# Optimization experiments

Measured on AMD Instinct MI355X. Metric: run time of the kernel, lower is better.

The kernel has to match this reference:

```python
import jax, jax.numpy as jnp
import numpy as np

B, T, D, H = 8, 1024, 1024, 16

def setup_inputs() -> dict:
    key = jax.random.key(0)
    k1, k2, k3, k4, k5 = jax.random.split(key, 5)
    x = jax.random.normal(k1, (B, T, D), dtype=jnp.float32)
    mask = jnp.tril(jnp.ones((T, T), dtype=bool))[None, None]  # [1,1,T,T] causal
    s = 0.02
    W_attn = jax.random.normal(k2, (D, 3 * D), dtype=jnp.float32) * s
    b_attn = jnp.zeros((3 * D,), dtype=jnp.float32)
    W_proj = jax.random.normal(k3, (D, D), dtype=jnp.float32) * s
    b_proj = jnp.zeros((D,), dtype=jnp.float32)
    return {"x": x, "mask": mask, "W_attn": W_attn, "b_attn": b_attn,
            "W_proj": W_proj, "b_proj": b_proj}

def reference(x, mask, W_attn, b_attn, W_proj, b_proj):
    num_heads = H
    b, t, d = x.shape
    hd = d // num_heads
    qkv = x @ W_attn + b_attn                      # [b,t,3d]
    q, k, v = jnp.split(qkv, 3, axis=-1)
    def to_heads(a):
        return a.reshape(b, t, num_heads, hd).transpose(0, 2, 1, 3)  # [b,h,t,hd]
    q, k, v = to_heads(q), to_heads(k), to_heads(v)
    scale = 1.0 / jnp.sqrt(jnp.float32(hd))
    attn = jnp.einsum('bhqd,bhkd->bhqk', q, k) * scale
    attn = jnp.where(mask, attn, jnp.finfo(jnp.float32).min)
    attn = jax.nn.softmax(attn, axis=-1)
    o = jnp.einsum('bhqk,bhkd->bhqd', attn, v)
    o = o.transpose(0, 2, 1, 3).reshape(b, t, d)   # [b,t,d]
    return o @ W_proj + b_proj
```

## Files before the change

### kernel.cpp

```cpp
#include <hip/hip_runtime.h>
#include <cstdint>


typedef __attribute__((ext_vector_type(8))) short bf16x8;
typedef __attribute__((ext_vector_type(4))) float f32x4;

__device__ __forceinline__ short f2b(float x) {
  unsigned u = __builtin_bit_cast(unsigned, x);
  u += 0x7fffu + ((u >> 16) & 1u);
  return (short)(u >> 16);
}

__device__ __forceinline__ void gl2lds16(short* l, const short* g) {
  __builtin_amdgcn_global_load_lds(
      (const __attribute__((address_space(1))) void*)g,
      (__attribute__((address_space(3))) void*)l, 16, 0, 0);
}


__global__ void f32_to_bf16_vec(const float* __restrict__ in,
                                short* __restrict__ outb, int n4) {
  int i = blockIdx.x * 256 + threadIdx.x;
  if (i >= n4) return;
  float4 v = ((const float4*)in)[i];
  short4 o;
  o.x = f2b(v.x); o.y = f2b(v.y); o.z = f2b(v.z); o.w = f2b(v.w);
  ((short4*)outb)[i] = o;
}

__global__ void transpose_f32_bf16(const float* __restrict__ in,
                                   short* __restrict__ out, int R, int C) {
  __shared__ float tile[32][33];
  int c0 = blockIdx.x * 32, r0 = blockIdx.y * 32;
  int tx = threadIdx.x, ty = threadIdx.y;
#pragma unroll
  for (int i = 0; i < 32; i += 8)
    tile[ty + i][tx] = in[(long)(r0 + ty + i) * C + c0 + tx];
  __syncthreads();
#pragma unroll
  for (int i = 0; i < 32; i += 8)
    out[(long)(c0 + ty + i) * R + r0 + tx] = f2b(tile[tx][ty + i]);
}


__global__ __launch_bounds__(512, 2) void gemm_qkv256(
    const short* __restrict__ A, const short* __restrict__ Bt,
    const float* __restrict__ bias,
    short* __restrict__ qh, short* __restrict__ kh, short* __restrict__ vT,
    int M, int N, int K) {
  __shared__ short As[2][256 * 64];
  __shared__ short Bs[2][256 * 64];
  const int t = threadIdx.x;
  const int wave = t >> 6, lane = t & 63;
  const int quad = lane >> 4, l15 = lane & 15;
  const int wm = wave >> 2, wn = wave & 3;

  const int nx = gridDim.x;
  const int bid0 = blockIdx.y * nx + blockIdx.x;
  const int cpx = (nx * gridDim.y) >> 3;
  const int bid = (bid0 & 7) * cpx + (bid0 >> 3);
  const int n0 = (bid % nx) * 256;
  const int m0 = (bid / nx) * 256;

  f32x4 acc[8][4] = {};

  const int srow = t >> 3;
  const int sch = (t & 7) ^ (srow & 7);
  const short* aS = A + (long)(m0 + srow) * K + sch * 8;
  const short* bS = Bt + (long)(n0 + srow) * K + sch * 8;
  const long rK = (long)64 * K;

  const int sw0 = (quad ^ (l15 & 7)) * 8;
  const int sw1 = ((4 + quad) ^ (l15 & 7)) * 8;
  const short* aF = &As[0][(wm * 128 + l15) * 64];
  const short* bF = &Bs[0][(wn * 64 + l15) * 64];
  const int BUF = 256 * 64;

  const int ntiles = K >> 6;

  {
    short* ad = &As[0][t * 8];
    short* bd = &Bs[0][t * 8];
    gl2lds16(bd, bS);
    gl2lds16(bd + 4096, bS + rK);
    gl2lds16(bd + 2 * 4096, bS + 2 * rK);
    gl2lds16(bd + 3 * 4096, bS + 3 * rK);
    gl2lds16(ad, aS);
    gl2lds16(ad + 2 * 4096, aS + 2 * rK);
    gl2lds16(ad + 4096, aS + rK);
    gl2lds16(ad + 3 * 4096, aS + 3 * rK);
  }
  asm volatile("s_waitcnt vmcnt(2)" ::: "memory");
  __builtin_amdgcn_s_barrier();

#pragma unroll 1
  for (int kt = 0; kt < ntiles - 1; ++kt) {
    const int cur = kt & 1;
    const short* Ab = aF + cur * BUF;
    const short* Bb = bF + cur * BUF;
    short* ad = &As[cur ^ 1][t * 8];
    short* bd = &Bs[cur ^ 1][t * 8];
    const short* aN = aS + (long)(kt + 1) * 64;
    const short* bN = bS + (long)(kt + 1) * 64;
#pragma unroll
    for (int ph = 0; ph < 4; ++ph) {
      const int mh = ph >> 1;
      const int sw = (ph & 1) ? sw1 : sw0;
      bf16x8 af[4], bf[4];
#pragma unroll
      for (int i = 0; i < 4; ++i)
        af[i] = *(const bf16x8*)(Ab + (mh * 64 + i * 16) * 64 + sw);
#pragma unroll
      for (int j = 0; j < 4; ++j)
        bf[j] = *(const bf16x8*)(Bb + j * 16 * 64 + sw);
      if (ph == 0) { gl2lds16(bd, bN); gl2lds16(bd + 4096, bN + rK); }
      if (ph == 1) { gl2lds16(bd + 2 * 4096, bN + 2 * rK);
                     gl2lds16(bd + 3 * 4096, bN + 3 * rK); }
      if (ph == 2) { gl2lds16(ad, aN); gl2lds16(ad + 2 * 4096, aN + 2 * rK); }
      if (ph == 3) { gl2lds16(ad + 4096, aN + rK);
                     gl2lds16(ad + 3 * 4096, aN + 3 * rK); }
      __builtin_amdgcn_s_barrier();
      asm volatile("s_waitcnt lgkmcnt(0)" ::: "memory");
      __builtin_amdgcn_sched_barrier(0);
      __builtin_amdgcn_s_setprio(1);
#pragma unroll
      for (int i = 0; i < 4; ++i)
#pragma unroll
        for (int j = 0; j < 4; ++j)
          acc[mh * 4 + i][j] = __builtin_amdgcn_mfma_f32_16x16x32_bf16(
              af[i], bf[j], acc[mh * 4 + i][j], 0, 0, 0);
      __builtin_amdgcn_s_setprio(0);
      if (ph == 1) asm volatile("s_waitcnt vmcnt(4)" ::: "memory");
      if (ph == 3) asm volatile("s_waitcnt vmcnt(2)" ::: "memory");
      __builtin_amdgcn_s_barrier();
    }
  }

  {
    const int cur = (ntiles - 1) & 1;
    const short* Ab = aF + cur * BUF;
    const short* Bb = bF + cur * BUF;
#pragma unroll
    for (int ph = 0; ph < 4; ++ph) {
      const int mh = ph >> 1;
      const int sw = (ph & 1) ? sw1 : sw0;
      bf16x8 af[4], bf[4];
#pragma unroll
      for (int i = 0; i < 4; ++i)
        af[i] = *(const bf16x8*)(Ab + (mh * 64 + i * 16) * 64 + sw);
#pragma unroll
      for (int j = 0; j < 4; ++j)
        bf[j] = *(const bf16x8*)(Bb + j * 16 * 64 + sw);
      __builtin_amdgcn_s_barrier();
      asm volatile("s_waitcnt lgkmcnt(0)" ::: "memory");
      __builtin_amdgcn_sched_barrier(0);
      __builtin_amdgcn_s_setprio(1);
#pragma unroll
      for (int i = 0; i < 4; ++i)
#pragma unroll
        for (int j = 0; j < 4; ++j)
          acc[mh * 4 + i][j] = __builtin_amdgcn_mfma_f32_16x16x32_bf16(
              af[i], bf[j], acc[mh * 4 + i][j], 0, 0, 0);
      __builtin_amdgcn_s_setprio(0);
      if (ph == 1) asm volatile("s_waitcnt vmcnt(0)" ::: "memory");
      __builtin_amdgcn_s_barrier();
    }
  }

  const int sec = n0 >> 10;
  const int b_ = m0 >> 10;
#pragma unroll
  for (int j = 0; j < 4; ++j) {
    int col = n0 + wn * 64 + j * 16 + l15;
    float bv = bias[col];
    int d = col & 1023, h = d >> 6, dh = d & 63;
    if (sec == 2) {
      long base = ((long)(b_ * 16 + h) * 64 + dh) * 1024;
#pragma unroll
      for (int i = 0; i < 8; ++i) {
        int tt0 = (m0 & 1023) + wm * 128 + i * 16 + quad * 4;
        short4 v;
        v.x = f2b(acc[i][j][0] + bv);
        v.y = f2b(acc[i][j][1] + bv);
        v.z = f2b(acc[i][j][2] + bv);
        v.w = f2b(acc[i][j][3] + bv);
        *(short4*)(vT + base + tt0) = v;
      }
    } else {
      short* dst = (sec == 0) ? qh : kh;
      long hbase = ((long)(b_ * 16 + h) * 1024) * 64 + dh;
#pragma unroll
      for (int i = 0; i < 8; ++i)
#pragma unroll
        for (int r = 0; r < 4; ++r) {
          int tt = (m0 & 1023) + wm * 128 + i * 16 + quad * 4 + r;
          dst[hbase + (long)tt * 64] = f2b(acc[i][j][r] + bv);
        }
    }
  }
}


__global__ __launch_bounds__(256, 3) void gemm_proj(
    const short* __restrict__ A, const short* __restrict__ Bt,
    const float* __restrict__ bias, float* __restrict__ outF,
    int M, int N, int K) {
  __shared__ short At[128 * 64];
  __shared__ short Bl[128 * 64];
  const int t = threadIdx.x;
  const int wave = t >> 6, lane = t & 63;
  const int quad = lane >> 4, l15 = lane & 15;
  const int wr = wave >> 1, wc = wave & 1;
  const int m0 = blockIdx.y * 128, n0 = blockIdx.x * 128;

  f32x4 acc[4][4] = {};

  const int srow = t >> 3;
  const int sch0 = t & 7;

  for (int k0 = 0; k0 < K; k0 += 64) {
    __syncthreads();
#pragma unroll
    for (int c = 0; c < 4; ++c) {
      int row = c * 32 + srow;
      int ch = sch0 ^ (row & 7);
      gl2lds16(At + (c * 256 + t) * 8, A + (long)(m0 + row) * K + k0 + ch * 8);
      gl2lds16(Bl + (c * 256 + t) * 8, Bt + (long)(n0 + row) * K + k0 + ch * 8);
    }
    asm volatile("s_waitcnt vmcnt(0)" ::: "memory");
    __syncthreads();

#pragma unroll
    for (int s = 0; s < 2; ++s) {
      const int cx = (s * 4 + quad) ^ (l15 & 7);
      bf16x8 af[4], bfr[4];
#pragma unroll
      for (int i = 0; i < 4; ++i)
        af[i] = *(const bf16x8*)(At + (wr * 64 + i * 16 + l15) * 64 + cx * 8);
#pragma unroll
      for (int j = 0; j < 4; ++j)
        bfr[j] = *(const bf16x8*)(Bl + (wc * 64 + j * 16 + l15) * 64 + cx * 8);
#pragma unroll
      for (int i = 0; i < 4; ++i)
#pragma unroll
        for (int j = 0; j < 4; ++j)
          acc[i][j] = __builtin_amdgcn_mfma_f32_16x16x32_bf16(af[i], bfr[j],
                                                              acc[i][j], 0, 0, 0);
    }
  }

#pragma unroll
  for (int j = 0; j < 4; ++j) {
    int col = n0 + wc * 64 + j * 16 + l15;
    float bv = bias[col];
#pragma unroll
    for (int i = 0; i < 4; ++i)
#pragma unroll
      for (int r = 0; r < 4; ++r) {
        int row = m0 + wr * 64 + i * 16 + quad * 4 + r;
        outF[(long)row * N + col] = acc[i][j][r] + bv;
      }
  }
}


__global__ __launch_bounds__(256, 2) void attn_kernel(
    const short* __restrict__ qh, const short* __restrict__ kh,
    const short* __restrict__ vT, short* __restrict__ attout) {
  __shared__ short Kb[2][64 * 64];
  __shared__ short Vb[2][64 * 64];
  __shared__ short P_lds[4][16][64];
  const int p = blockIdx.x;
  const int bh = blockIdx.y;
  const int t = threadIdx.x;
  const int wave = t >> 6, lane = t & 63, quad = lane >> 4, l15 = lane & 15;
  const short* q_head = qh + (long)bh * 1024 * 64;
  const short* k_head = kh + (long)bh * 1024 * 64;
  const short* v_head = vT + (long)bh * 64 * 1024;
  const int b_ = bh >> 4, h_ = bh & 15;
  const float sl = 0.125f * 1.44269504089f;

  const int qt[4] = {p, 7 - p, 8 + p, 15 - p};

  auto stage = [&](int kt, int buf) {
    const int kk0 = kt * 64;
#pragma unroll
    for (int i = 0; i < 2; ++i) {
      int s = i * 256 + t;
      int row = s >> 3, cg = (s & 7) ^ (row & 7);
      gl2lds16(&Kb[buf][s * 8], k_head + (kk0 + row) * 64 + cg * 8);
    }
#pragma unroll
    for (int i = 0; i < 2; ++i) {
      int s = i * 256 + t;
      int row = s >> 3, cg = (s & 7) ^ (row & 7);
      gl2lds16(&Vb[buf][s * 8], v_head + row * 1024 + kk0 + cg * 8);
    }
  };

  bf16x8 qf[4][2];
#pragma unroll
  for (int i = 0; i < 4; ++i) {
    int qb = qt[i] * 64 + wave * 16;
#pragma unroll
    for (int s = 0; s < 2; ++s)
      qf[i][s] = *(const bf16x8*)(q_head + (qb + l15) * 64 + s * 32 + quad * 8);
  }

  float l[4][4] = {};
  f32x4 o[4][4] = {};

  stage(0, 0);
  __syncthreads();

  const int nkt = qt[3] + 1;

#pragma unroll 1
  for (int kt = 0; kt < nkt; ++kt) {
    const int buf = kt & 1;
    const short* Kt = Kb[buf];
    const short* Vt = Vb[buf];

    bf16x8 kfr[4][2], vfr[4][2];
#pragma unroll
    for (int jj = 0; jj < 4; ++jj) {
      int row = jj * 16 + l15;
#pragma unroll
      for (int s = 0; s < 2; ++s) {
        int off = ((s * 4 + quad) ^ (row & 7)) * 8;
        kfr[jj][s] = *(const bf16x8*)(Kt + row * 64 + off);
        vfr[jj][s] = *(const bf16x8*)(Vt + row * 64 + off);
      }
    }

    if (kt + 1 < nkt) stage(kt + 1, buf ^ 1);

#pragma unroll
    for (int i = 0; i < 4; ++i) {
      if (kt <= qt[i]) {
        f32x4 s4[4] = {};
#pragma unroll
        for (int jj = 0; jj < 4; ++jj) {
          s4[jj] = __builtin_amdgcn_mfma_f32_16x16x32_bf16(qf[i][0], kfr[jj][0],
                                                           s4[jj], 0, 0, 0);
          s4[jj] = __builtin_amdgcn_mfma_f32_16x16x32_bf16(qf[i][1], kfr[jj][1],
                                                           s4[jj], 0, 0, 0);
        }
        const bool diag = (kt == qt[i]);
        const int qb = qt[i] * 64 + wave * 16;
#pragma unroll
        for (int jj = 0; jj < 4; ++jj) {
          int key = kt * 64 + jj * 16 + l15;
          int ch = jj * 2 + (l15 >> 3), co = l15 & 7;
#pragma unroll
          for (int r = 0; r < 4; ++r) {
            int row = quad * 4 + r;
            float sv = s4[jj][r] * sl;
            if (diag && key > qb + row) sv = -1e30f;
            float e = __builtin_amdgcn_exp2f(sv);
            l[i][r] += e;
            P_lds[wave][row][(ch ^ (row & 7)) * 8 + co] = f2b(e);
          }
        }
        asm volatile("s_waitcnt lgkmcnt(0)" ::: "memory");
        bf16x8 pf[2];
#pragma unroll
        for (int s = 0; s < 2; ++s)
          pf[s] =
              *(const bf16x8*)(&P_lds[wave][l15][((s * 4 + quad) ^ (l15 & 7)) * 8]);
#pragma unroll
        for (int dj = 0; dj < 4; ++dj) {
          o[i][dj] = __builtin_amdgcn_mfma_f32_16x16x32_bf16(pf[0], vfr[dj][0],
                                                             o[i][dj], 0, 0, 0);
          o[i][dj] = __builtin_amdgcn_mfma_f32_16x16x32_bf16(pf[1], vfr[dj][1],
                                                             o[i][dj], 0, 0, 0);
        }
      }
    }
    __syncthreads();
  }

#pragma unroll
  for (int off = 1; off < 16; off <<= 1)
#pragma unroll
    for (int i = 0; i < 4; ++i)
#pragma unroll
      for (int r = 0; r < 4; ++r) l[i][r] += __shfl_xor(l[i][r], off);

  const int erow = lane >> 3, ech = lane & 7;
#pragma unroll
  for (int i = 0; i < 4; ++i) {
    float inv[4];
#pragma unroll
    for (int r = 0; r < 4; ++r) inv[r] = __builtin_amdgcn_rcpf(l[i][r]);
    const int qb = qt[i] * 64 + wave * 16;
#pragma unroll
    for (int dj = 0; dj < 4; ++dj) {
      int ch = dj * 2 + (l15 >> 3), co = l15 & 7;
#pragma unroll
      for (int r = 0; r < 4; ++r) {
        int row = quad * 4 + r;
        P_lds[wave][row][(ch ^ (row & 7)) * 8 + co] = f2b(o[i][dj][r] * inv[r]);
      }
    }
    asm volatile("s_waitcnt lgkmcnt(0)" ::: "memory");
#pragma unroll
    for (int pass = 0; pass < 2; ++pass) {
      int row = pass * 8 + erow;
      bf16x8 v = *(const bf16x8*)(&P_lds[wave][row][(ech ^ (row & 7)) * 8]);
      long g = (long)b_ * 1024 + qb + row;
      *(bf16x8*)(attout + g * 1024 + h_ * 64 + ech * 8) = v;
    }
    asm volatile("s_waitcnt lgkmcnt(0)" ::: "memory");
  }
}


extern "C" void kernel_launch(void* const* d_in, const int* in_sizes, int n_in,
                              void* d_out, int out_size, void* d_ws,
                              size_t ws_size, hipStream_t stream) {
  const float* x = (const float*)d_in[0];
  const float* W_attn = (const float*)d_in[2];
  const float* b_attn = (const float*)d_in[3];
  const float* W_proj = (const float*)d_in[4];
  const float* b_proj = (const float*)d_in[5];
  float* out = (float*)d_out;

  char* ws = (char*)d_ws;
  const size_t MB = 1u << 20;
  short* xb = (short*)(ws);
  short* WaT = (short*)(ws + 16 * MB);
  short* WpT = (short*)(ws + 22 * MB);
  short* qh = (short*)(ws + 24 * MB);
  short* kh = (short*)(ws + 40 * MB);
  short* vT = (short*)(ws + 56 * MB);
  short* attout = xb;

  f32_to_bf16_vec<<<8192, 256, 0, stream>>>(x, xb, 2097152);
  transpose_f32_bf16<<<dim3(3072 / 32, 1024 / 32), dim3(32, 8), 0, stream>>>(
      W_attn, WaT, 1024, 3072);
  transpose_f32_bf16<<<dim3(1024 / 32, 1024 / 32), dim3(32, 8), 0, stream>>>(
      W_proj, WpT, 1024, 1024);
  gemm_qkv256<<<dim3(3072 / 256, 8192 / 256), 512, 0, stream>>>(
      xb, WaT, b_attn, qh, kh, vT, 8192, 3072, 1024);
  attn_kernel<<<dim3(4, 128), 256, 0, stream>>>(qh, kh, vT, attout);
  gemm_proj<<<dim3(1024 / 128, 8192 / 128), 256, 0, stream>>>(
      attout, WpT, b_proj, out, 8192, 1024, 1024);
}
```

Before: 240.8 us.

## Switch QKV GEMM to a four-stage K=32 LDS pipeline with three tiles in flight

Replaces the double-buffered K=64 shared-memory tiles in the QKV projection GEMM with four K=32 buffers, keeping three tiles of global-to-LDS loads in flight. The goal is to hide more global load latency behind the MFMA work. The total LDS footprint stays the same. The swizzle changes to suit 32-wide rows, and tile-dependent vmcnt waits handle the prologue and epilogue. The cost is twice as many loop iterations, with the barriers and waits that come with each.

```diff
diff --git a/kernel.cpp b/kernel.cpp
--- a/kernel.cpp
+++ b/kernel.cpp
@@ -15,6 +15,18 @@
   __builtin_amdgcn_global_load_lds(
       (const __attribute__((address_space(1))) void*)g,
       (__attribute__((address_space(3))) void*)l, 16, 0, 0);
+}
+
+template <int N>
+struct IC {
+  static constexpr int value = N;
+};
+
+template <int N>
+__device__ __forceinline__ void waitvm() {
+  if constexpr (N == 8) asm volatile("s_waitcnt vmcnt(8)" ::: "memory");
+  else if constexpr (N == 4) asm volatile("s_waitcnt vmcnt(4)" ::: "memory");
+  else if constexpr (N == 0) asm volatile("s_waitcnt vmcnt(0)" ::: "memory");
 }
 
 
@@ -48,8 +60,8 @@
     const float* __restrict__ bias,
     short* __restrict__ qh, short* __restrict__ kh, short* __restrict__ vT,
     int M, int N, int K) {
-  __shared__ short As[2][256 * 64];
-  __shared__ short Bs[2][256 * 64];
+  __shared__ short As[4][256 * 32];
+  __shared__ short Bs[4][256 * 32];
   const int t = threadIdx.x;
   const int wave = t >> 6, lane = t & 63;
   const int quad = lane >> 4, l15 = lane & 15;
@@ -64,108 +76,84 @@
 
   f32x4 acc[8][4] = {};
 
-  const int srow = t >> 3;
-  const int sch = (t & 7) ^ (srow & 7);
-  const short* aS = A + (long)(m0 + srow) * K + sch * 8;
-  const short* bS = Bt + (long)(n0 + srow) * K + sch * 8;
-  const long rK = (long)64 * K;
-
-  const int sw0 = (quad ^ (l15 & 7)) * 8;
-  const int sw1 = ((4 + quad) ^ (l15 & 7)) * 8;
-  const short* aF = &As[0][(wm * 128 + l15) * 64];
-  const short* bF = &Bs[0][(wn * 64 + l15) * 64];
-  const int BUF = 256 * 64;
-
-  const int ntiles = K >> 6;
-
-  {
-    short* ad = &As[0][t * 8];
-    short* bd = &Bs[0][t * 8];
-    gl2lds16(bd, bS);
-    gl2lds16(bd + 4096, bS + rK);
-    gl2lds16(bd + 2 * 4096, bS + 2 * rK);
-    gl2lds16(bd + 3 * 4096, bS + 3 * rK);
-    gl2lds16(ad, aS);
-    gl2lds16(ad + 2 * 4096, aS + 2 * rK);
-    gl2lds16(ad + 4096, aS + rK);
-    gl2lds16(ad + 3 * 4096, aS + 3 * rK);
-  }
-  asm volatile("s_waitcnt vmcnt(2)" ::: "memory");
+  const int srow = t >> 2;
+  const int sck = (t & 3) ^ ((t >> 2) & 3) ^ ((t >> 4) & 3);
+  const short* aS = A + (long)(m0 + srow) * K + sck * 8;
+  const short* bS = Bt + (long)(n0 + srow) * K + sck * 8;
+  const long rK = (long)128 * K;
+
+  const int cx = quad ^ (l15 & 3) ^ ((l15 >> 2) & 3);
+  const int arow0 = wm * 128 + l15;
+  const int brow0 = wn * 64 + l15;
+
+  const int NT = K >> 5;
+
+  auto issueA = [&](int kt) {
+    short* d = &As[kt & 3][t * 8];
+    const short* s = aS + (long)kt * 32;
+    gl2lds16(d, s);
+    gl2lds16(d + 4096, s + rK);
+  };
+  auto issueB = [&](int kt) {
+    short* d = &Bs[kt & 3][t * 8];
+    const short* s = bS + (long)kt * 32;
+    gl2lds16(d, s);
+    gl2lds16(d + 4096, s + rK);
+  };
+
+  issueA(0); issueB(0);
+  issueA(1); issueB(1);
+  issueA(2); issueB(2);
+  asm volatile("s_waitcnt vmcnt(8)" ::: "memory");
   __builtin_amdgcn_s_barrier();
 
+  auto tile = [&](int kt, auto wc, bool issue) {
+    const short* Ab = As[kt & 3];
+    const short* Bb = Bs[kt & 3];
+    bf16x8 af[4], bf[4];
+#pragma unroll
+    for (int i = 0; i < 4; ++i)
+      af[i] = *(const bf16x8*)(Ab + (arow0 + i * 16) * 32 + cx * 8);
+#pragma unroll
+    for (int j = 0; j < 4; ++j)
+      bf[j] = *(const bf16x8*)(Bb + (brow0 + j * 16) * 32 + cx * 8);
+    if (issue) issueA(kt + 3);
+    __builtin_amdgcn_s_barrier();
+    asm volatile("s_waitcnt lgkmcnt(0)" ::: "memory");
+    __builtin_amdgcn_sched_barrier(0);
+    __builtin_amdgcn_s_setprio(1);
+#pragma unroll
+    for (int i = 0; i < 4; ++i)
+#pragma unroll
+      for (int j = 0; j < 4; ++j)
+        acc[i][j] = __builtin_amdgcn_mfma_f32_16x16x32_bf16(af[i], bf[j],
+                                                            acc[i][j], 0, 0, 0);
+    __builtin_amdgcn_s_setprio(0);
+    __builtin_amdgcn_s_barrier();
+#pragma unroll
+    for (int i = 0; i < 4; ++i)
+      af[i] = *(const bf16x8*)(Ab + (arow0 + 64 + i * 16) * 32 + cx * 8);
+    if (issue) issueB(kt + 3);
+    __builtin_amdgcn_s_barrier();
+    asm volatile("s_waitcnt lgkmcnt(0)" ::: "memory");
+    __builtin_amdgcn_sched_barrier(0);
+    __builtin_amdgcn_s_setprio(1);
+#pragma unroll
+    for (int i = 0; i < 4; ++i)
+#pragma unroll
+      for (int j = 0; j < 4; ++j)
+        acc[4 + i][j] = __builtin_amdgcn_mfma_f32_16x16x32_bf16(
+            af[i], bf[j], acc[4 + i][j], 0, 0, 0);
+    __builtin_amdgcn_s_setprio(0);
+    waitvm<decltype(wc)::value>();
+    __builtin_amdgcn_s_barrier();
+  };
+
 #pragma unroll 1
-  for (int kt = 0; kt < ntiles - 1; ++kt) {
-    const int cur = kt & 1;
-    const short* Ab = aF + cur * BUF;
-    const short* Bb = bF + cur * BUF;
-    short* ad = &As[cur ^ 1][t * 8];
-    short* bd = &Bs[cur ^ 1][t * 8];
-    const short* aN = aS + (long)(kt + 1) * 64;
-    const short* bN = bS + (long)(kt + 1) * 64;
-#pragma unroll
-    for (int ph = 0; ph < 4; ++ph) {
-      const int mh = ph >> 1;
-      const int sw = (ph & 1) ? sw1 : sw0;
-      bf16x8 af[4], bf[4];
-#pragma unroll
-      for (int i = 0; i < 4; ++i)
-        af[i] = *(const bf16x8*)(Ab + (mh * 64 + i * 16) * 64 + sw);
-#pragma unroll
-      for (int j = 0; j < 4; ++j)
-        bf[j] = *(const bf16x8*)(Bb + j * 16 * 64 + sw);
-      if (ph == 0) { gl2lds16(bd, bN); gl2lds16(bd + 4096, bN + rK); }
-      if (ph == 1) { gl2lds16(bd + 2 * 4096, bN + 2 * rK);
-                     gl2lds16(bd + 3 * 4096, bN + 3 * rK); }
-      if (ph == 2) { gl2lds16(ad, aN); gl2lds16(ad + 2 * 4096, aN + 2 * rK); }
-      if (ph == 3) { gl2lds16(ad + 4096, aN + rK);
-                     gl2lds16(ad + 3 * 4096, aN + 3 * rK); }
-      __builtin_amdgcn_s_barrier();
-      asm volatile("s_waitcnt lgkmcnt(0)" ::: "memory");
-      __builtin_amdgcn_sched_barrier(0);
-      __builtin_amdgcn_s_setprio(1);
-#pragma unroll
-      for (int i = 0; i < 4; ++i)
-#pragma unroll
-        for (int j = 0; j < 4; ++j)
-          acc[mh * 4 + i][j] = __builtin_amdgcn_mfma_f32_16x16x32_bf16(
-              af[i], bf[j], acc[mh * 4 + i][j], 0, 0, 0);
-      __builtin_amdgcn_s_setprio(0);
-      if (ph == 1) asm volatile("s_waitcnt vmcnt(4)" ::: "memory");
-      if (ph == 3) asm volatile("s_waitcnt vmcnt(2)" ::: "memory");
-      __builtin_amdgcn_s_barrier();
-    }
-  }
-
-  {
-    const int cur = (ntiles - 1) & 1;
-    const short* Ab = aF + cur * BUF;
-    const short* Bb = bF + cur * BUF;
-#pragma unroll
-    for (int ph = 0; ph < 4; ++ph) {
-      const int mh = ph >> 1;
-      const int sw = (ph & 1) ? sw1 : sw0;
-      bf16x8 af[4], bf[4];
-#pragma unroll
-      for (int i = 0; i < 4; ++i)
-        af[i] = *(const bf16x8*)(Ab + (mh * 64 + i * 16) * 64 + sw);
-#pragma unroll
-      for (int j = 0; j < 4; ++j)
-        bf[j] = *(const bf16x8*)(Bb + j * 16 * 64 + sw);
-      __builtin_amdgcn_s_barrier();
-      asm volatile("s_waitcnt lgkmcnt(0)" ::: "memory");
-      __builtin_amdgcn_sched_barrier(0);
-      __builtin_amdgcn_s_setprio(1);
-#pragma unroll
-      for (int i = 0; i < 4; ++i)
-#pragma unroll
-        for (int j = 0; j < 4; ++j)
-          acc[mh * 4 + i][j] = __builtin_amdgcn_mfma_f32_16x16x32_bf16(
-              af[i], bf[j], acc[mh * 4 + i][j], 0, 0, 0);
-      __builtin_amdgcn_s_setprio(0);
-      if (ph == 1) asm volatile("s_waitcnt vmcnt(0)" ::: "memory");
-      __builtin_amdgcn_s_barrier();
-    }
-  }
+  for (int kt = 0; kt < NT - 3; ++kt) tile(kt, IC<8>{}, true);
+  tile(NT - 3, IC<4>{}, false);
+  tile(NT - 2, IC<0>{}, false);
+  tile(NT - 1, IC<-1>{}, false);
 
   const int sec = n0 >> 10;
   const int b_ = m0 >> 10;
```

After: 258.5 us. +7.3%, slower.
